# Optimization experiments

Measured on AMD Instinct MI355X. Metric: run time of the kernel, lower is better.

## Reference

```python
import jax, jax.numpy as jnp
import numpy as np

S_SIGMA = 8      # spatial downsampling of the bilateral grid
N_BINS = 16      # intensity bins (range resolution)
EPS = 1e-8


def _blur_axis(g, k, axis):
    """1D correlation of grid g with small tap filter k along `axis` (zero pad)."""
    taps = k.shape[0]
    r = taps // 2
    pad = [(0, 0)] * g.ndim
    pad[axis] = (r, r)
    gp = jnp.pad(g, pad)
    n = g.shape[axis]
    out = k[0] * jax.lax.slice_in_dim(gp, 0, n, axis=axis)
    for i in range(1, taps):
        out = out + k[i] * jax.lax.slice_in_dim(gp, i, i + n, axis=axis)
    return out


def _bilateral_one(img, fs, fr):
    """Bilateral grid splat -> blur -> slice for a single [H,W] channel.
    Guide signal is the channel itself (values assumed in [0,1])."""
    H, W = img.shape
    GH = (H - 1) // S_SIGMA + 2
    GW = (W - 1) // S_SIGMA + 2
    GZ = N_BINS + 1

    ys = jnp.arange(H, dtype=img.dtype)
    xs = jnp.arange(W, dtype=img.dtype)

    # ---- splat (nearest-cell scatter-add of homogeneous (value, weight)) ----
    gy = jnp.round(ys / S_SIGMA).astype(jnp.int32)            # [H]
    gx = jnp.round(xs / S_SIGMA).astype(jnp.int32)            # [W]
    gyg, gxg = jnp.meshgrid(gy, gx, indexing='ij')            # [H,W]
    gz = jnp.clip(jnp.round(img * (N_BINS - 1)), 0, N_BINS - 1).astype(jnp.int32)
    val = jnp.zeros((GH, GW, GZ), img.dtype).at[gyg, gxg, gz].add(img)
    wt = jnp.zeros((GH, GW, GZ), img.dtype).at[gyg, gxg, gz].add(jnp.ones_like(img))

    # ---- blur grid: learnable 5-tap filter_s along y,x and filter_r along z ----
    for axis, k in ((0, fs), (1, fs), (2, fr)):
        val = _blur_axis(val, k, axis)
        wt = _blur_axis(wt, k, axis)

    # ---- slice (trilinear gather at (y/s, x/s, I*(NB-1))) ----
    fy = ys / S_SIGMA
    fx = xs / S_SIGMA
    fz = jnp.clip(img * (N_BINS - 1), 0.0, N_BINS - 1)        # [H,W]
    y0 = jnp.floor(fy).astype(jnp.int32)
    x0 = jnp.floor(fx).astype(jnp.int32)
    z0 = jnp.floor(fz).astype(jnp.int32)
    y1 = jnp.minimum(y0 + 1, GH - 1)
    x1 = jnp.minimum(x0 + 1, GW - 1)
    z1 = jnp.minimum(z0 + 1, GZ - 1)
    ty = fy - y0.astype(img.dtype)                            # [H]
    tx = fx - x0.astype(img.dtype)                            # [W]
    tz = fz - z0.astype(img.dtype)                            # [H,W]

    out_v = jnp.zeros_like(img)
    out_w = jnp.zeros_like(img)
    for yi, wy in ((y0, 1.0 - ty), (y1, ty)):
        for xi, wx in ((x0, 1.0 - tx), (x1, tx)):
            for zi, wz in ((z0, 1.0 - tz), (z1, tz)):
                w = wy[:, None] * wx[None, :] * wz            # [H,W]
                out_v = out_v + w * val[yi[:, None], xi[None, :], zi]
                out_w = out_w + w * wt[yi[:, None], xi[None, :], zi]
    return out_v / (out_w + EPS)


def setup_inputs() -> dict:
    key = jax.random.key(0)
    k1, k2 = jax.random.split(key)
    blurred_batch = jax.random.uniform(k1, (4, 3, 1024, 1024), dtype=jnp.float32)
    kernel_batch = jax.random.uniform(k2, (4, 11, 11), dtype=jnp.float32)
    g = jnp.array([1.0, 4.0, 6.0, 4.0, 1.0], dtype=jnp.float32)
    g = g / g.sum()  # smooth 5-tap filter so the blur is nontrivial
    return {
        'blurred_batch': blurred_batch,
        'kernel_batch': kernel_batch,
        'filter_s': g,
        'filter_r': g,
        'num_irls_iter': 1,
        'num_cg_iter': 5,
    }


def reference(blurred_batch, kernel_batch, filter_s, filter_r, num_irls_iter, num_cg_iter):
    # kernel_batch, num_irls_iter, num_cg_iter are unused on this code path,
    # matching the original forward (only BilateralGrid.apply touches x).
    B, C, H, W = blurred_batch.shape
    imgs = blurred_batch.reshape(B * C, H, W)
    out = jax.vmap(lambda im: _bilateral_one(im, filter_s, filter_r))(imgs)
    return out.reshape(B, C, H, W)
```

## Files before the change

### kernel.cpp

```cpp
#include <hip/hip_runtime.h>
#include <hip/hip_fp16.h>

#define S_SIGMA 8
#define NBINS   16
#define HDIM    1024
#define WDIM    1024
#define GH      129
#define GW      129
#define GZ      17
#define CELLS   (GH*GW*GZ)
#define ROWSZ   (GW*GZ)
#define EPSV    1e-8f
#define PKONE   (1u << 25)
#define PKMASK  0x1FFFFFFu
#define PKSCL   4096.0f
#define PKINV   (1.0f/4096.0f)


__device__ __forceinline__ int xcd_swizzle(int orig, int nwg) {
    int q = nwg >> 3, r = nwg & 7;
    int xcd = orig & 7, off = orig >> 3;
    return (xcd < r ? xcd * (q + 1) : r * (q + 1) + (xcd - r) * q) + off;
}


__global__ __launch_bounds__(256) void splat_gather_kernel(
    const float* __restrict__ img, __half2* __restrict__ grid, int nImg, int imgBase,
    int nBlocks)
{
    __shared__ unsigned lbin[16 * 64];

    int tid = threadIdx.x;
    int c   = tid & 63;
    int q   = tid >> 6;
    int blk = xcd_swizzle(blockIdx.x, nBlocks);
    int cellIdx = blk * 64 + c;
    int total = nImg * GH * GW;

    for (int i = tid; i < 16 * 64; i += 256) lbin[i] = 0u;
    __syncthreads();

    if (cellIdx < total) {
        int b   = cellIdx / (GH * GW);
        int rem = cellIdx - b * (GH * GW);
        int gy  = rem / GW;
        int gx  = rem - gy * GW;
        const float* ib = img + (size_t)(imgBase + b) * (HDIM * WDIM);

        bool interior = (gx >= 1) & (gx <= 127) & (gy >= 1) & (gy <= 127);
        if (interior) {
            int py = gy & 1, px = gx & 1;
            int ylo = 8 * gy - 4 + py;
            int nr  = 9 - 2 * py;
            int ax  = 8 * gx - 4;
            for (int r = q; r < nr; r += 4) {
                const float* rp = ib + (size_t)(ylo + r) * WDIM + ax;
                float4 A = *(const float4*)rp;
                float4 B = *(const float4*)(rp + 4);
                float  cv = rp[8];
                float e7[7] = {A.y, A.z, A.w, B.x, B.y, B.z, B.w};
                #pragma unroll
                for (int j = 0; j < 7; ++j) {
                    float v = e7[j];
                    int gz = min(max((int)rintf(v * 15.0f), 0), 15);
                    atomicAdd(&lbin[gz * 64 + c], PKONE + (unsigned)rintf(v * PKSCL));
                }
                if (!px) {
                    int gz = min(max((int)rintf(A.x * 15.0f), 0), 15);
                    atomicAdd(&lbin[gz * 64 + c], PKONE + (unsigned)rintf(A.x * PKSCL));
                    gz = min(max((int)rintf(cv * 15.0f), 0), 15);
                    atomicAdd(&lbin[gz * 64 + c], PKONE + (unsigned)rintf(cv * PKSCL));
                }
            }
        } else {
            int ylo = max(0, 8 * gy - 4 + (gy & 1));
            int yhi = min(HDIM - 1, 8 * gy + 4 - (gy & 1));
            int xlo = max(0, 8 * gx - 4 + (gx & 1));
            int xhi = min(WDIM - 1, 8 * gx + 4 - (gx & 1));
            for (int y = ylo + q; y <= yhi; y += 4) {
                const float* row = ib + (size_t)y * WDIM;
                for (int x = xlo; x <= xhi; ++x) {
                    float v = row[x];
                    int gz = min(max((int)rintf(v * 15.0f), 0), 15);
                    atomicAdd(&lbin[gz * 64 + c], PKONE + (unsigned)rintf(v * PKSCL));
                }
            }
        }
    }
    __syncthreads();

    if (cellIdx < total) {
        __half2* dst = grid + (size_t)cellIdx * GZ;
        int zlo = q * 4;
        int zhi = (q == 3) ? 17 : zlo + 4;
        for (int z = zlo; z < zhi; ++z) {
            float vx = 0.f, vy = 0.f;
            if (z != 16) {
                unsigned w = lbin[z * 64 + c];
                vx = (float)(w & PKMASK) * PKINV;
                vy = (float)(w >> 25);
            }
            dst[z] = __floats2half2_rn(vx, vy);
        }
    }
}

#define NRI 9

__global__ __launch_bounds__(256) void blur_yxz_row(
    const __half2* __restrict__ in, __half2* __restrict__ out,
    const float* __restrict__ kfs, const float* __restrict__ kfr)
{
    __shared__ float2 sbin[ROWSZ];

    int tid = threadIdx.x;
    int gy  = xcd_swizzle(blockIdx.x, GH);
    int b   = blockIdx.y;

    float ks[5] = {kfs[0], kfs[1], kfs[2], kfs[3], kfs[4]};
    float kr[5] = {kfr[0], kfr[1], kfr[2], kfr[3], kfr[4]};

    const __half2* gb = in + (size_t)b * CELLS;
    float2 st[NRI];
    #pragma unroll
    for (int it = 0; it < NRI; ++it) {
        int i = tid + it * 256;
        float2 a; a.x = 0.f; a.y = 0.f;
        if (i < ROWSZ) {
            #pragma unroll
            for (int t = 0; t < 5; ++t) {
                int yy = gy + t - 2;
                if (yy >= 0 && yy < GH) {
                    float2 g = __half22float2(gb[(size_t)yy * ROWSZ + i]);
                    a.x += ks[t] * g.x;
                    a.y += ks[t] * g.y;
                }
            }
        }
        st[it] = a;
    }
    #pragma unroll
    for (int it = 0; it < NRI; ++it) {
        int i = tid + it * 256;
        if (i < ROWSZ) sbin[i] = st[it];
    }
    __syncthreads();

    float2 rt[NRI];
    #pragma unroll
    for (int it = 0; it < NRI; ++it) {
        int o = tid + it * 256;
        float2 a; a.x = 0.f; a.y = 0.f;
        if (o < ROWSZ) {
            int gx = o / GZ;
            #pragma unroll
            for (int t = 0; t < 5; ++t) {
                int xx = gx + t - 2;
                if (xx >= 0 && xx < GW) {
                    float2 g = sbin[o + (t - 2) * GZ];
                    a.x += ks[t] * g.x;
                    a.y += ks[t] * g.y;
                }
            }
        }
        rt[it] = a;
    }
    __syncthreads();
    #pragma unroll
    for (int it = 0; it < NRI; ++it) {
        int o = tid + it * 256;
        if (o < ROWSZ) sbin[o] = rt[it];
    }
    __syncthreads();

    __half2* ob = out + (size_t)b * CELLS + (size_t)gy * ROWSZ;
    for (int o2 = tid; o2 < ROWSZ; o2 += 256) {
        int z  = o2 / GW;
        int gx = o2 - z * GW;
        float ax = 0.f, ay = 0.f;
        #pragma unroll
        for (int t = 0; t < 5; ++t) {
            int zz = z + t - 2;
            if (zz >= 0 && zz < GZ) {
                float2 g = sbin[gx * GZ + zz];
                ax += kr[t] * g.x;
                ay += kr[t] * g.y;
            }
        }
        ob[o2] = __floats2half2_rn(ax, ay);
    }
}

#define XP2   136
#define RST   XP2
#define ZST   (2*XP2)

__global__ __launch_bounds__(256) void slice_rows_kernel(
    const float* __restrict__ img, const __half2* __restrict__ grid,
    float* __restrict__ out, int imgBase)
{
    __shared__ float2 sg[GZ * ZST];

    int tid = threadIdx.x;
    int k   = xcd_swizzle(blockIdx.x, HDIM / 8);
    int b   = blockIdx.y;

    const __half2* gsrc = grid + (size_t)b * CELLS + (size_t)k * ROWSZ;
    for (int i = tid; i < 2 * ROWSZ; i += 256) {
        int r   = i / ROWSZ;
        int rem = i - r * ROWSZ;
        int z   = rem / GW;
        int x0  = rem - z * GW;
        sg[z * ZST + r * RST + x0] = __half22float2(gsrc[i]);
    }
    __syncthreads();

    int x   = tid << 2;
    int x0v = tid >> 1;
    float txb = (float)(x & 7) * 0.125f;

    size_t rowBase = (size_t)(imgBase + b) * (HDIM * WDIM) + (size_t)(k << 3) * WDIM + x;

    #pragma unroll
    for (int r = 0; r < 8; ++r) {
        size_t pixBase = rowBase + (size_t)r * WDIM;
        float4 v4 = *(const float4*)(img + pixBase);
        float ty = (float)r * 0.125f;
        float wy0 = 1.f - ty, wy1 = ty;

        float vv[4] = {v4.x, v4.y, v4.z, v4.w};
        float rr[4];
        #pragma unroll
        for (int j = 0; j < 4; ++j) {
            float v  = vv[j];
            float fz = fminf(fmaxf(v * 15.0f, 0.0f), 15.0f);
            float zf = floorf(fz);
            int   z0 = (int)zf;
            float tz = fz - zf;
            float tx = txb + (float)j * 0.125f;
            float wx0 = 1.f - tx, wx1 = tx;
            float wz0 = 1.f - tz, wz1 = tz;

            int base = z0 * ZST + x0v;
            float2 g000 = sg[base];
            float2 g010 = sg[base + 1];
            float2 g100 = sg[base + RST];
            float2 g110 = sg[base + RST + 1];
            float2 g001 = sg[base + ZST];
            float2 g011 = sg[base + ZST + 1];
            float2 g101 = sg[base + ZST + RST];
            float2 g111 = sg[base + ZST + RST + 1];

            float ov = 0.f, ow = 0.f, w;
            w = wy0 * wx0 * wz0; ov += w * g000.x; ow += w * g000.y;
            w = wy0 * wx0 * wz1; ov += w * g001.x; ow += w * g001.y;
            w = wy0 * wx1 * wz0; ov += w * g010.x; ow += w * g010.y;
            w = wy0 * wx1 * wz1; ov += w * g011.x; ow += w * g011.y;
            w = wy1 * wx0 * wz0; ov += w * g100.x; ow += w * g100.y;
            w = wy1 * wx0 * wz1; ov += w * g101.x; ow += w * g101.y;
            w = wy1 * wx1 * wz0; ov += w * g110.x; ow += w * g110.y;
            w = wy1 * wx1 * wz1; ov += w * g111.x; ow += w * g111.y;
            rr[j] = ov / (ow + EPSV);
        }
        float4 r4; r4.x = rr[0]; r4.y = rr[1]; r4.z = rr[2]; r4.w = rr[3];
        *(float4*)(out + pixBase) = r4;
    }
}

extern "C" void kernel_launch(void* const* d_in, const int* in_sizes, int n_in,
                              void* d_out, int out_size, void* d_ws, size_t ws_size,
                              hipStream_t stream)
{
    const float* img = (const float*)d_in[0];
    const float* fs  = (const float*)d_in[2];
    const float* fr  = (const float*)d_in[3];
    float* out = (float*)d_out;

    int nImgTotal = in_sizes[0] / (HDIM * WDIM);
    size_t perImgBytes = (size_t)CELLS * sizeof(__half2);

    int maxChunk = (int)(ws_size / (2 * perImgBytes));
    if (maxChunk < 1) return;
    if (maxChunk > nImgTotal) maxChunk = nImgTotal;

    for (int base = 0; base < nImgTotal; base += maxChunk) {
        int c = nImgTotal - base;
        if (c > maxChunk) c = maxChunk;

        __half2* A = (__half2*)d_ws;
        __half2* B = A + (size_t)c * CELLS;

        int nCells = c * GH * GW;
        int cellBlocks = (nCells + 63) / 64;
        splat_gather_kernel<<<cellBlocks, 256, 0, stream>>>(img, A, c, base, cellBlocks);

        dim3 bgrid(GH, c);
        blur_yxz_row<<<bgrid, 256, 0, stream>>>(A, B, fs, fr);

        dim3 sgrid(HDIM / 8, c);
        slice_rows_kernel<<<sgrid, 256, 0, stream>>>(img, B, out, base);
    }
}
```

Before: 85.02 us.

## Split blur row blocks into two x-halves with halo columns

Each blur block now handles half of a grid row along x, loading a 2-column halo so the x-blur stays correct, and the launch grid doubles to 2*GH blocks per image. This gives more blocks, better occupancy and a smaller shared-memory footprint, and cuts per-thread register arrays from 9 to 5 entries. The cost is some redundant y-blur work on the halo columns and a more complex output indexing pattern.

Result: no change. 86.63 us (+1.9%).

```diff
diff --git a/kernel.cpp b/kernel.cpp
--- a/kernel.cpp
+++ b/kernel.cpp
@@ -105,28 +105,38 @@
     }
 }
 
-#define NRI 9
+#define NST_MAX (67*GZ)
+#define NRI2 5
 
 __global__ __launch_bounds__(256) void blur_yxz_row(
     const __half2* __restrict__ in, __half2* __restrict__ out,
     const float* __restrict__ kfs, const float* __restrict__ kfr)
 {
-    __shared__ float2 sbin[ROWSZ];
+    __shared__ float2 sbin[NST_MAX];
 
     int tid = threadIdx.x;
-    int gy  = xcd_swizzle(blockIdx.x, GH);
+    int gyh = xcd_swizzle(blockIdx.x, 2 * GH);
+    int gy  = gyh >> 1;
+    int h   = gyh & 1;
     int b   = blockIdx.y;
+
+    int gxs  = h ? 63 : 0;
+    int ncol = h ? 66 : 67;
+    int nst  = ncol * GZ;
+    int olo  = h ? 2 : 0;
+    int ocnt = h ? 64 : 65;
+    int gxo  = h ? 65 : 0;
 
     float ks[5] = {kfs[0], kfs[1], kfs[2], kfs[3], kfs[4]};
     float kr[5] = {kfr[0], kfr[1], kfr[2], kfr[3], kfr[4]};
 
-    const __half2* gb = in + (size_t)b * CELLS;
-    float2 st[NRI];
-    #pragma unroll
-    for (int it = 0; it < NRI; ++it) {
+    const __half2* gb = in + (size_t)b * CELLS + (size_t)gxs * GZ;
+    float2 st[NRI2];
+    #pragma unroll
+    for (int it = 0; it < NRI2; ++it) {
         int i = tid + it * 256;
         float2 a; a.x = 0.f; a.y = 0.f;
-        if (i < ROWSZ) {
+        if (i < nst) {
             #pragma unroll
             for (int t = 0; t < 5; ++t) {
                 int yy = gy + t - 2;
@@ -140,24 +150,25 @@
         st[it] = a;
     }
     #pragma unroll
-    for (int it = 0; it < NRI; ++it) {
+    for (int it = 0; it < NRI2; ++it) {
         int i = tid + it * 256;
-        if (i < ROWSZ) sbin[i] = st[it];
-    }
-    __syncthreads();
-
-    float2 rt[NRI];
-    #pragma unroll
-    for (int it = 0; it < NRI; ++it) {
+        if (i < nst) sbin[i] = st[it];
+    }
+    __syncthreads();
+
+    float2 rt[NRI2];
+    #pragma unroll
+    for (int it = 0; it < NRI2; ++it) {
         int o = tid + it * 256;
         float2 a; a.x = 0.f; a.y = 0.f;
-        if (o < ROWSZ) {
-            int gx = o / GZ;
+        if (o < nst) {
+            int lx = o / GZ;
             #pragma unroll
             for (int t = 0; t < 5; ++t) {
-                int xx = gx + t - 2;
-                if (xx >= 0 && xx < GW) {
-                    float2 g = sbin[o + (t - 2) * GZ];
+                int xg = gxs + lx + t - 2;
+                int lo = o + (t - 2) * GZ;
+                if (xg >= 0 && xg < GW && lo >= 0 && lo < nst) {
+                    float2 g = sbin[lo];
                     a.x += ks[t] * g.x;
                     a.y += ks[t] * g.y;
                 }
@@ -167,27 +178,29 @@
     }
     __syncthreads();
     #pragma unroll
-    for (int it = 0; it < NRI; ++it) {
+    for (int it = 0; it < NRI2; ++it) {
         int o = tid + it * 256;
-        if (o < ROWSZ) sbin[o] = rt[it];
-    }
-    __syncthreads();
-
-    __half2* ob = out + (size_t)b * CELLS + (size_t)gy * ROWSZ;
-    for (int o2 = tid; o2 < ROWSZ; o2 += 256) {
-        int z  = o2 / GW;
-        int gx = o2 - z * GW;
+        if (o < nst) sbin[o] = rt[it];
+    }
+    __syncthreads();
+
+    __half2* ob = out + (size_t)b * CELLS + (size_t)gy * ROWSZ + gxo;
+    int nout = ocnt * GZ;
+    for (int o2 = tid; o2 < nout; o2 += 256) {
+        int z  = o2 / ocnt;
+        int j  = o2 - z * ocnt;
+        int cb = (olo + j) * GZ;
         float ax = 0.f, ay = 0.f;
         #pragma unroll
         for (int t = 0; t < 5; ++t) {
             int zz = z + t - 2;
             if (zz >= 0 && zz < GZ) {
-                float2 g = sbin[gx * GZ + zz];
+                float2 g = sbin[cb + zz];
                 ax += kr[t] * g.x;
                 ay += kr[t] * g.y;
             }
         }
-        ob[o2] = __floats2half2_rn(ax, ay);
+        ob[(size_t)z * GW + j] = __floats2half2_rn(ax, ay);
     }
 }
 
@@ -294,7 +307,7 @@
         int cellBlocks = (nCells + 63) / 64;
         splat_gather_kernel<<<cellBlocks, 256, 0, stream>>>(img, A, c, base, cellBlocks);
 
-        dim3 bgrid(GH, c);
+        dim3 bgrid(2 * GH, c);
         blur_yxz_row<<<bgrid, 256, 0, stream>>>(A, B, fs, fr);
 
         dim3 sgrid(HDIM / 8, c);
```
